# Kernel optimization log

Measured on AMD Instinct MI355X. Metric: run time of the kernel, lower is better.

## Reference

```python
import jax, jax.numpy as jnp
import numpy as np

HEADS = 8

def setup_inputs() -> dict:
    key = jax.random.key(0)
    k1, k2, k3, k4 = jax.random.split(key, 4)
    B, C_IN, H, W = 16, 256, 64, 64
    C_OUT = 256
    s = 1.0 / np.sqrt(C_IN)
    x = jax.random.normal(k1, (B, C_IN, H, W), dtype=jnp.float32)
    wq = jax.random.normal(k2, (C_OUT, C_IN), dtype=jnp.float32) * s
    wk = jax.random.normal(k3, (C_OUT, C_IN), dtype=jnp.float32) * s
    wv = jax.random.normal(k4, (C_OUT, C_IN), dtype=jnp.float32) * s
    return {"x": x, "wq": wq, "wk": wk, "wv": wv}

def _feat(t):
    # ELU(x) + 1  (positive feature map for linear attention)
    return jax.nn.elu(t) + 1.0

def reference(x, wq, wk, wv):
    B, C, H, W = x.shape
    M = H * W
    c_out = wq.shape[0]
    dh = c_out // HEADS
    scale = 1.0 / np.sqrt(dh)
    xf = x.reshape(B, C, M)  # flatten spatial
    # 1x1 conv (no bias) == channel matmul; reshape to [B, heads, dh, M]
    def proj(w):
        return jnp.einsum('oc,bcm->bom', w, xf).reshape(B, HEADS, dh, M)
    q = _feat(proj(wq)) * scale
    k = _feat(proj(wk)) * scale
    v = proj(wv)
    # linear attention: KV = k v^T over spatial, then apply to q
    KV = jnp.einsum('bhcm,bhdm->bhcd', k, v)          # [B,h,dh,dh]
    out = jnp.einsum('bhcd,bhcm->bhdm', KV, q)        # [B,h,dh,M]
    k_sum = k.sum(axis=-1)                             # [B,h,dh]
    denom = jnp.einsum('bhcm,bhc->bhm', q, k_sum)      # [B,h,M]
    denom = jnp.maximum(denom, 1e-6)[:, :, None, :]
    out = out / denom
    return out.reshape(B, c_out, H, W)
```

## Files before the change

### kernel.cpp

```cpp
#include <hip/hip_runtime.h>
#include <hip/hip_bf16.h>


typedef __attribute__((ext_vector_type(8))) short bf16x8;
typedef __attribute__((ext_vector_type(4))) float f32x4;
typedef __attribute__((ext_vector_type(4))) unsigned int u32x4;
typedef __attribute__((ext_vector_type(4))) float float4v;

#define DEVI static __device__ __forceinline__

DEVI unsigned short f2bf(float f){
  __hip_bfloat16 h = __float2bfloat16(f);
  return __builtin_bit_cast(unsigned short, h);
}
DEVI unsigned int pk2(float a, float b){
  return (unsigned int)f2bf(a) | ((unsigned int)f2bf(b) << 16);
}
DEVI float feat(float p){
  return (p > 0.f ? p + 1.f : __expf(p)) * 0.17677669529663687f;
}

DEVI f32x4 mfma16(u32x4 a, u32x4 b, f32x4 c){
  return __builtin_amdgcn_mfma_f32_16x16x32_bf16(
      __builtin_bit_cast(bf16x8, a), __builtin_bit_cast(bf16x8, b), c, 0, 0, 0);
}

DEVI int swz8(int m){ return ((m ^ (m >> 3)) & 7) << 4; }

typedef __attribute__((address_space(3))) unsigned int as3_u32;
typedef __attribute__((address_space(1))) const unsigned int as1_u32;
DEVI void gload16(const void* g, void* l){
  __builtin_amdgcn_global_load_lds((as1_u32*)g, (as3_u32*)l, 16, 0, 0);
}
DEVI void stage_tile(const char* src, void* buf, int w, int lane){
  #pragma unroll
  for (int i = 0; i < 4; ++i){
    int ub = w * 1024 + i * 8192;
    gload16(src + ub + lane * 16, (char*)buf + ub);
  }
}

DEVI void stage_load(const float* __restrict__ xb, int m0, int tid, float4v* r){
  #pragma unroll
  for (int it = 0; it < 2; ++it){
    int cq = (tid >> 4) + it * 32;
    int mq = tid & 15;
    const float* p = xb + (size_t)(cq * 4) * 4096 + m0 + mq * 4;
    r[it*4+0] = *(const float4v*)(p);
    r[it*4+1] = *(const float4v*)(p + 4096);
    r[it*4+2] = *(const float4v*)(p + 8192);
    r[it*4+3] = *(const float4v*)(p + 12288);
  }
}
DEVI void stage_write(unsigned short* xT, int tid, const float4v* r){
  #pragma unroll
  for (int it = 0; it < 2; ++it){
    int cq = (tid >> 4) + it * 32;
    int mq = tid & 15;
    int c0 = cq * 4, ml0 = mq * 4;
    #pragma unroll
    for (int j = 0; j < 4; ++j){
      int m = ml0 + j;
      unsigned int lo = pk2(r[it*4+0][j], r[it*4+1][j]);
      unsigned int hi = pk2(r[it*4+2][j], r[it*4+3][j]);
      int off = m * 512 + ((c0 * 2) ^ swz8(m));
      unsigned long long v = (unsigned long long)lo | ((unsigned long long)hi << 32);
      *(unsigned long long*)((char*)xT + off) = v;
    }
  }
}
DEVI void dump_tile_sw(const unsigned short* xT, unsigned short* dst, int tid){
  #pragma unroll
  for (int i = 0; i < 4; ++i){
    int f = i * 512 + tid;
    int lane = f & 63, nt = (f >> 6) & 3, kk = f >> 8;
    int m = nt * 16 + (lane & 15);
    int col = (kk * 64 + (lane >> 4) * 16) ^ swz8(m);
    u32x4 v = *(const u32x4*)((const char*)xT + m * 512 + col);
    *(u32x4*)((char*)dst + (size_t)f * 16) = v;
  }
}

__global__ void wconv(const float* __restrict__ wq, const float* __restrict__ wk,
                      const float* __restrict__ wv,
                      unsigned short* __restrict__ wkvf, unsigned short* __restrict__ wqf){
  int t = blockIdx.x * 256 + threadIdx.x;
  if (t < 16384){
    int lane = t & 63, kk = (t >> 6) & 7, ot = (t >> 9) & 3, h = t >> 11;
    int l15 = lane & 15, hi = lane >> 4;
    const float* src = (ot < 2) ? (wk + (size_t)(h * 32 + ot * 16 + l15) * 256)
                                : (wv + (size_t)(h * 32 + (ot - 2) * 16 + l15) * 256);
    src += kk * 32 + hi * 8;
    unsigned short* dst = wkvf + (size_t)t * 8;
    #pragma unroll
    for (int j = 0; j < 8; ++j) dst[j] = f2bf(src[j]);
  } else if (t < 24576){
    int u = t - 16384;
    int lane = u & 63, kk = (u >> 6) & 7, ot = (u >> 9) & 1, h = u >> 10;
    int l15 = lane & 15, hi = lane >> 4;
    const float* src = wq + (size_t)(h * 32 + ot * 16 + l15) * 256 + kk * 32 + hi * 8;
    unsigned short* dst = wqf + (size_t)u * 8;
    #pragma unroll
    for (int j = 0; j < 8; ++j) dst[j] = f2bf(src[j]);
  }
}

DEVI void compute_sub_sw(const unsigned short* __restrict__ xT,
                         const unsigned short* __restrict__ wkvf,
                         int w, int l15, int hi, int lane,
                         f32x4 (&kvacc)[2][2], f32x4 (&ksacc)[2], u32x4 ones){
  #pragma unroll
  for (int g = 0; g < 2; ++g){
    f32x4 acc[2][4];
    #pragma unroll
    for (int a1 = 0; a1 < 2; ++a1)
      #pragma unroll
      for (int a2 = 0; a2 < 4; ++a2) acc[a1][a2] = f32x4{0.f,0.f,0.f,0.f};

    #pragma unroll
    for (int kk = 0; kk < 8; ++kk){
      u32x4 xf[2];
      #pragma unroll
      for (int n2 = 0; n2 < 2; ++n2){
        int m = (g * 2 + n2) * 16 + l15;
        xf[n2] = *(const u32x4*)((const char*)xT + m * 512 + ((kk * 64 + hi * 16) ^ swz8(m)));
      }
      #pragma unroll
      for (int ot = 0; ot < 4; ++ot){
        u32x4 wf = *(const u32x4*)(wkvf + ((((size_t)w * 4 + ot) * 8 + kk) * 64 + lane) * 8);
        #pragma unroll
        for (int n2 = 0; n2 < 2; ++n2) acc[n2][ot] = mfma16(xf[n2], wf, acc[n2][ot]);
      }
    }
    u32x4 kf[2], vf[2];
    #pragma unroll
    for (int t2 = 0; t2 < 2; ++t2){
      kf[t2][0] = pk2(feat(acc[0][t2][0]), feat(acc[0][t2][1]));
      kf[t2][1] = pk2(feat(acc[0][t2][2]), feat(acc[0][t2][3]));
      kf[t2][2] = pk2(feat(acc[1][t2][0]), feat(acc[1][t2][1]));
      kf[t2][3] = pk2(feat(acc[1][t2][2]), feat(acc[1][t2][3]));
      vf[t2][0] = pk2(acc[0][t2+2][0], acc[0][t2+2][1]);
      vf[t2][1] = pk2(acc[0][t2+2][2], acc[0][t2+2][3]);
      vf[t2][2] = pk2(acc[1][t2+2][0], acc[1][t2+2][1]);
      vf[t2][3] = pk2(acc[1][t2+2][2], acc[1][t2+2][3]);
    }
    #pragma unroll
    for (int ct = 0; ct < 2; ++ct){
      #pragma unroll
      for (int dt = 0; dt < 2; ++dt)
        kvacc[ct][dt] = mfma16(kf[ct], vf[dt], kvacc[ct][dt]);
      ksacc[ct] = mfma16(kf[ct], ones, ksacc[ct]);
    }
  }
}

__global__ void __launch_bounds__(512) xkv(const float* __restrict__ x,
        const unsigned short* __restrict__ wkvf,
        unsigned short* __restrict__ ximg,
        float* __restrict__ kvp, float* __restrict__ ksp){
  __shared__ __align__(16) unsigned short xT[2][16384];
  const int tid = threadIdx.x, lane = tid & 63, w = tid >> 6;
  const int l15 = lane & 15, hi = lane >> 4;
  const int ch = blockIdx.x, b = blockIdx.y;
  const float* xb = x + (size_t)b * (256 * 4096);
  unsigned short* img = ximg + ((size_t)b * 64 + ch * 2) * 16384;

  f32x4 kvacc[2][2];
  f32x4 ksacc[2];
  #pragma unroll
  for (int i = 0; i < 2; ++i){
    ksacc[i] = f32x4{0.f,0.f,0.f,0.f};
    #pragma unroll
    for (int j = 0; j < 2; ++j) kvacc[i][j] = f32x4{0.f,0.f,0.f,0.f};
  }
  u32x4 ones = {0u,0u,0u,0u};
  if (l15 == 0){ ones[0] = ones[1] = ones[2] = ones[3] = 0x3f803f80u; }

  float4v rs[8];
  stage_load(xb, ch * 128, tid, rs);
  stage_write(xT[0], tid, rs);
  __syncthreads();
  stage_load(xb, ch * 128 + 64, tid, rs);
  compute_sub_sw(xT[0], wkvf, w, l15, hi, lane, kvacc, ksacc, ones);
  dump_tile_sw(xT[0], img, tid);
  stage_write(xT[1], tid, rs);
  __syncthreads();
  compute_sub_sw(xT[1], wkvf, w, l15, hi, lane, kvacc, ksacc, ones);
  dump_tile_sw(xT[1], img + 16384, tid);

  size_t base = (((size_t)b * 32 + ch) * 8 + w) * 1024;
  #pragma unroll
  for (int ct = 0; ct < 2; ++ct){
    #pragma unroll
    for (int dt = 0; dt < 2; ++dt){
      #pragma unroll
      for (int r = 0; r < 4; ++r){
        int c = ct * 16 + hi * 4 + r, d = dt * 16 + l15;
        kvp[base + c * 32 + d] = kvacc[ct][dt][r];
      }
    }
  }
  if (l15 == 0){
    size_t kb = (((size_t)b * 32 + ch) * 8 + w) * 32;
    #pragma unroll
    for (int ct = 0; ct < 2; ++ct)
      #pragma unroll
      for (int r = 0; r < 4; ++r) ksp[kb + ct * 16 + hi * 4 + r] = ksacc[ct][r];
  }
}

__global__ void k_red(const float* __restrict__ kvp, const float* __restrict__ ksp,
                      unsigned short* __restrict__ kvt, unsigned short* __restrict__ ksb){
  int t = blockIdx.x * 256 + threadIdx.x;
  int dq = t & 7;
  int c  = (t >> 3) & 31;
  int h  = (t >> 8) & 7;
  int b  = t >> 11;
  float4v s = {0.f,0.f,0.f,0.f};
  for (int c2 = 0; c2 < 32; ++c2){
    const float* p = kvp + ((((size_t)b * 32 + c2) * 8 + h) * 1024) + c * 32 + dq * 4;
    float4v r = *(const float4v*)p;
    s.x += r.x; s.y += r.y; s.z += r.z; s.w += r.w;
  }
  int pos = ((c >> 2) & 3) * 8 + ((c >> 4) << 2) + (c & 3);
  unsigned short* q = kvt + ((size_t)b * 8 + h) * 1024;
  q[(dq * 4 + 0) * 32 + pos] = f2bf(s.x);
  q[(dq * 4 + 1) * 32 + pos] = f2bf(s.y);
  q[(dq * 4 + 2) * 32 + pos] = f2bf(s.z);
  q[(dq * 4 + 3) * 32 + pos] = f2bf(s.w);
  if (dq == 0){
    float ks = 0.f;
    for (int c2 = 0; c2 < 32; ++c2)
      ks += ksp[(((size_t)b * 32 + c2) * 8 + h) * 32 + c];
    ksb[((size_t)b * 8 + h) * 32 + pos] = f2bf(ks);
  }
}

DEVI void q_sub(const unsigned short* __restrict__ xT,
                const unsigned short* __restrict__ wqf,
                u32x4 afkv0, u32x4 afkv1, u32x4 afd,
                int w, int l15, int hi, int lane, float* __restrict__ ob){
  f32x4 qa[2][4];
  #pragma unroll
  for (int a1 = 0; a1 < 2; ++a1)
    #pragma unroll
    for (int a2 = 0; a2 < 4; ++a2) qa[a1][a2] = f32x4{0.f,0.f,0.f,0.f};

  #pragma unroll
  for (int kk = 0; kk < 8; ++kk){
    u32x4 xf[4];
    #pragma unroll
    for (int nt = 0; nt < 4; ++nt)
      xf[nt] = *(const u32x4*)(xT + (((size_t)kk * 4 + nt) * 64 + lane) * 8);
    #pragma unroll
    for (int ot = 0; ot < 2; ++ot){
      u32x4 wf = *(const u32x4*)(wqf + ((((size_t)w * 2 + ot) * 8 + kk) * 64 + lane) * 8);
      #pragma unroll
      for (int nt = 0; nt < 4; ++nt) qa[ot][nt] = mfma16(wf, xf[nt], qa[ot][nt]);
    }
  }

  #pragma unroll
  for (int nt = 0; nt < 4; ++nt){
    u32x4 bq;
    bq[0] = pk2(feat(qa[0][nt][0]), feat(qa[0][nt][1]));
    bq[1] = pk2(feat(qa[0][nt][2]), feat(qa[0][nt][3]));
    bq[2] = pk2(feat(qa[1][nt][0]), feat(qa[1][nt][1]));
    bq[3] = pk2(feat(qa[1][nt][2]), feat(qa[1][nt][3]));

    f32x4 o0 = {0.f,0.f,0.f,0.f}, o1 = {0.f,0.f,0.f,0.f}, dn = {0.f,0.f,0.f,0.f};
    o0 = mfma16(afkv0, bq, o0);
    o1 = mfma16(afkv1, bq, o1);
    dn = mfma16(afd, bq, dn);
    float dv = __shfl(dn[0], l15, 64);
    float inv = 1.0f / fmaxf(dv, 1e-6f);
    #pragma unroll
    for (int r = 0; r < 4; ++r){
      ob[(size_t)(hi * 4 + r) * 4096 + nt * 16 + l15]      = o0[r] * inv;
      ob[(size_t)(16 + hi * 4 + r) * 4096 + nt * 16 + l15] = o1[r] * inv;
    }
  }
}

__global__ void __launch_bounds__(512) k_q(const unsigned short* __restrict__ ximg,
        const unsigned short* __restrict__ wqf,
        const unsigned short* __restrict__ kvt,
        const unsigned short* __restrict__ ksb,
        float* __restrict__ out){
  __shared__ __align__(16) unsigned short xT[2][16384];
  const int tid = threadIdx.x, lane = tid & 63, w = tid >> 6;
  const int l15 = lane & 15, hi = lane >> 4;
  const int ch = blockIdx.x, b = blockIdx.y;
  const char* src = (const char*)(ximg + ((size_t)b * 64 + ch * 2) * 16384);

  size_t kvbase = ((size_t)b * 8 + w) * 1024;
  u32x4 afkv0 = *(const u32x4*)(kvt + kvbase + (size_t)l15 * 32 + hi * 8);
  u32x4 afkv1 = *(const u32x4*)(kvt + kvbase + (size_t)(16 + l15) * 32 + hi * 8);
  u32x4 afd = {0u,0u,0u,0u};
  if (l15 == 0) afd = *(const u32x4*)(ksb + ((size_t)b * 8 + w) * 32 + hi * 8);

  stage_tile(src, xT[0], w, lane);
  __syncthreads();
  stage_tile(src + 32768, xT[1], w, lane);

  float* ob = out + ((size_t)b * 256 + w * 32) * 4096 + ch * 128;
  q_sub(xT[0], wqf, afkv0, afkv1, afd, w, l15, hi, lane, ob);
  __syncthreads();
  q_sub(xT[1], wqf, afkv0, afkv1, afd, w, l15, hi, lane, ob + 64);
}

extern "C" void kernel_launch(void* const* d_in, const int* in_sizes, int n_in,
                              void* d_out, int out_size, void* d_ws, size_t ws_size,
                              hipStream_t stream) {
  const float* x  = (const float*)d_in[0];
  const float* wq = (const float*)d_in[1];
  const float* wk = (const float*)d_in[2];
  const float* wv = (const float*)d_in[3];
  float* out = (float*)d_out;
  char* ws = (char*)d_ws;

  unsigned short* wkvf = (unsigned short*)(ws);
  unsigned short* wqf  = (unsigned short*)(ws + 262144);
  unsigned short* kvt  = (unsigned short*)(ws + 393216);
  unsigned short* ksb  = (unsigned short*)(ws + 655360);
  float* kvp = (float*)(ws + 1048576);
  float* ksp = (float*)(ws + 17825792);
  unsigned short* ximg = (unsigned short*)(ws + 18350080);

  hipLaunchKernelGGL(wconv, dim3(96), dim3(256), 0, stream, wq, wk, wv, wkvf, wqf);
  hipLaunchKernelGGL(xkv,   dim3(32, 16), dim3(512), 0, stream, x, wkvf, ximg, kvp, ksp);
  hipLaunchKernelGGL(k_red, dim3(128), dim3(256), 0, stream, kvp, ksp, kvt, ksb);
  hipLaunchKernelGGL(k_q,   dim3(32, 16), dim3(512), 0, stream, ximg, wqf, kvt, ksb, out);
}
```

Before: 70.80 us.

## Recompute bf16 x tile in query kernel instead of dumping intermediate image

Removes the bf16 copy of x that the KV kernel wrote to workspace and the query kernel read back. Instead, the query kernel reloads fp32 x, converts it to bf16 into swizzled LDS, and reads MFMA fragments through the swizzle. This cuts one intermediate write and its read but doubles the bytes the query kernel fetches from x. It also replaces the asynchronous global-to-LDS copy with register staging and conversion.

```diff
diff --git a/kernel.cpp b/kernel.cpp
--- a/kernel.cpp
+++ b/kernel.cpp
@@ -26,19 +26,6 @@
 }
 
 DEVI int swz8(int m){ return ((m ^ (m >> 3)) & 7) << 4; }
-
-typedef __attribute__((address_space(3))) unsigned int as3_u32;
-typedef __attribute__((address_space(1))) const unsigned int as1_u32;
-DEVI void gload16(const void* g, void* l){
-  __builtin_amdgcn_global_load_lds((as1_u32*)g, (as3_u32*)l, 16, 0, 0);
-}
-DEVI void stage_tile(const char* src, void* buf, int w, int lane){
-  #pragma unroll
-  for (int i = 0; i < 4; ++i){
-    int ub = w * 1024 + i * 8192;
-    gload16(src + ub + lane * 16, (char*)buf + ub);
-  }
-}
 
 DEVI void stage_load(const float* __restrict__ xb, int m0, int tid, float4v* r){
   #pragma unroll
@@ -67,17 +54,6 @@
       unsigned long long v = (unsigned long long)lo | ((unsigned long long)hi << 32);
       *(unsigned long long*)((char*)xT + off) = v;
     }
-  }
-}
-DEVI void dump_tile_sw(const unsigned short* xT, unsigned short* dst, int tid){
-  #pragma unroll
-  for (int i = 0; i < 4; ++i){
-    int f = i * 512 + tid;
-    int lane = f & 63, nt = (f >> 6) & 3, kk = f >> 8;
-    int m = nt * 16 + (lane & 15);
-    int col = (kk * 64 + (lane >> 4) * 16) ^ swz8(m);
-    u32x4 v = *(const u32x4*)((const char*)xT + m * 512 + col);
-    *(u32x4*)((char*)dst + (size_t)f * 16) = v;
   }
 }
 
@@ -156,14 +132,12 @@
 
 __global__ void __launch_bounds__(512) xkv(const float* __restrict__ x,
         const unsigned short* __restrict__ wkvf,
-        unsigned short* __restrict__ ximg,
         float* __restrict__ kvp, float* __restrict__ ksp){
   __shared__ __align__(16) unsigned short xT[2][16384];
   const int tid = threadIdx.x, lane = tid & 63, w = tid >> 6;
   const int l15 = lane & 15, hi = lane >> 4;
   const int ch = blockIdx.x, b = blockIdx.y;
   const float* xb = x + (size_t)b * (256 * 4096);
-  unsigned short* img = ximg + ((size_t)b * 64 + ch * 2) * 16384;
 
   f32x4 kvacc[2][2];
   f32x4 ksacc[2];
@@ -182,11 +156,9 @@
   __syncthreads();
   stage_load(xb, ch * 128 + 64, tid, rs);
   compute_sub_sw(xT[0], wkvf, w, l15, hi, lane, kvacc, ksacc, ones);
-  dump_tile_sw(xT[0], img, tid);
   stage_write(xT[1], tid, rs);
   __syncthreads();
   compute_sub_sw(xT[1], wkvf, w, l15, hi, lane, kvacc, ksacc, ones);
-  dump_tile_sw(xT[1], img + 16384, tid);
 
   size_t base = (((size_t)b * 32 + ch) * 8 + w) * 1024;
   #pragma unroll
@@ -236,10 +208,10 @@
   }
 }
 
-DEVI void q_sub(const unsigned short* __restrict__ xT,
-                const unsigned short* __restrict__ wqf,
-                u32x4 afkv0, u32x4 afkv1, u32x4 afd,
-                int w, int l15, int hi, int lane, float* __restrict__ ob){
+DEVI void q_sub_sw(const unsigned short* __restrict__ xT,
+                   const unsigned short* __restrict__ wqf,
+                   u32x4 afkv0, u32x4 afkv1, u32x4 afd,
+                   int w, int l15, int hi, int lane, float* __restrict__ ob){
   f32x4 qa[2][4];
   #pragma unroll
   for (int a1 = 0; a1 < 2; ++a1)
@@ -250,8 +222,10 @@
   for (int kk = 0; kk < 8; ++kk){
     u32x4 xf[4];
     #pragma unroll
-    for (int nt = 0; nt < 4; ++nt)
-      xf[nt] = *(const u32x4*)(xT + (((size_t)kk * 4 + nt) * 64 + lane) * 8);
+    for (int nt = 0; nt < 4; ++nt){
+      int m = nt * 16 + l15;
+      xf[nt] = *(const u32x4*)((const char*)xT + m * 512 + ((kk * 64 + hi * 16) ^ swz8(m)));
+    }
     #pragma unroll
     for (int ot = 0; ot < 2; ++ot){
       u32x4 wf = *(const u32x4*)(wqf + ((((size_t)w * 2 + ot) * 8 + kk) * 64 + lane) * 8);
@@ -282,7 +256,7 @@
   }
 }
 
-__global__ void __launch_bounds__(512) k_q(const unsigned short* __restrict__ ximg,
+__global__ void __launch_bounds__(512) k_q(const float* __restrict__ x,
         const unsigned short* __restrict__ wqf,
         const unsigned short* __restrict__ kvt,
         const unsigned short* __restrict__ ksb,
@@ -291,7 +265,7 @@
   const int tid = threadIdx.x, lane = tid & 63, w = tid >> 6;
   const int l15 = lane & 15, hi = lane >> 4;
   const int ch = blockIdx.x, b = blockIdx.y;
-  const char* src = (const char*)(ximg + ((size_t)b * 64 + ch * 2) * 16384);
+  const float* xb = x + (size_t)b * (256 * 4096);
 
   size_t kvbase = ((size_t)b * 8 + w) * 1024;
   u32x4 afkv0 = *(const u32x4*)(kvt + kvbase + (size_t)l15 * 32 + hi * 8);
@@ -299,14 +273,17 @@
   u32x4 afd = {0u,0u,0u,0u};
   if (l15 == 0) afd = *(const u32x4*)(ksb + ((size_t)b * 8 + w) * 32 + hi * 8);
 
-  stage_tile(src, xT[0], w, lane);
+  float4v rs[8];
+  stage_load(xb, ch * 128, tid, rs);
+  stage_write(xT[0], tid, rs);
   __syncthreads();
-  stage_tile(src + 32768, xT[1], w, lane);
+  stage_load(xb, ch * 128 + 64, tid, rs);
 
   float* ob = out + ((size_t)b * 256 + w * 32) * 4096 + ch * 128;
-  q_sub(xT[0], wqf, afkv0, afkv1, afd, w, l15, hi, lane, ob);
+  q_sub_sw(xT[0], wqf, afkv0, afkv1, afd, w, l15, hi, lane, ob);
+  stage_write(xT[1], tid, rs);
   __syncthreads();
-  q_sub(xT[1], wqf, afkv0, afkv1, afd, w, l15, hi, lane, ob + 64);
+  q_sub_sw(xT[1], wqf, afkv0, afkv1, afd, w, l15, hi, lane, ob + 64);
 }
 
 extern "C" void kernel_launch(void* const* d_in, const int* in_sizes, int n_in,
@@ -325,10 +302,9 @@
   unsigned short* ksb  = (unsigned short*)(ws + 655360);
   float* kvp = (float*)(ws + 1048576);
   float* ksp = (float*)(ws + 17825792);
-  unsigned short* ximg = (unsigned short*)(ws + 18350080);
 
   hipLaunchKernelGGL(wconv, dim3(96), dim3(256), 0, stream, wq, wk, wv, wkvf, wqf);
-  hipLaunchKernelGGL(xkv,   dim3(32, 16), dim3(512), 0, stream, x, wkvf, ximg, kvp, ksp);
+  hipLaunchKernelGGL(xkv,   dim3(32, 16), dim3(512), 0, stream, x, wkvf, kvp, ksp);
   hipLaunchKernelGGL(k_red, dim3(128), dim3(256), 0, stream, kvp, ksp, kvt, ksb);
-  hipLaunchKernelGGL(k_q,   dim3(32, 16), dim3(512), 0, stream, ximg, wqf, kvt, ksb, out);
-}
+  hipLaunchKernelGGL(k_q,   dim3(32, 16), dim3(512), 0, stream, x, wqf, kvt, ksb, out);
+}
```

Result: slower. 77.61 us (+9.6%).
